# Optimization experiments

Measured on AMD Instinct MI355X. Metric: run time of the kernel, lower is better.

The kernel has to match this reference:

```python
import jax, jax.numpy as jnp
import numpy as np

NUM_GRAPHS = 512
NODES_PER_GRAPH = 152  # hard-coded by reshape(-1, 152*C) in the original forward
DEG = 8
N = NUM_GRAPHS * NODES_PER_GRAPH          # 77824
E = NUM_GRAPHS * NODES_PER_GRAPH * DEG    # 622592
F_IN = 128
HID = 32
HEADS = 6
C = HID * HEADS                           # 192
EPS = 1e-5
NEG_SLOPE = 0.2


def setup_inputs() -> dict:
    key = jax.random.key(0)
    ks = jax.random.split(key, 20)
    x = jax.random.normal(ks[0], (N, F_IN), dtype=jnp.float32)
    # edges are intra-graph: local indices in [0,152) + per-graph offset
    src_l = jax.random.randint(ks[1], (E,), 0, NODES_PER_GRAPH)
    dst_l = jax.random.randint(ks[2], (E,), 0, NODES_PER_GRAPH)
    offs = (jnp.arange(E) // (NODES_PER_GRAPH * DEG)) * NODES_PER_GRAPH
    edge_index = jnp.stack([src_l + offs, dst_l + offs]).astype(jnp.int32)
    batch = (jnp.arange(N) // NODES_PER_GRAPH).astype(jnp.int32)

    def g(k, shape, s=0.05):
        return jax.random.normal(k, shape, dtype=jnp.float32) * s

    return {
        "x": x, "edge_index": edge_index, "batch": batch,
        # GATConv 1: in=128 -> heads=6, d_head=32, concat -> 192
        "W1": g(ks[3], (F_IN, C)), "a_src1": g(ks[4], (HEADS, HID)),
        "a_dst1": g(ks[5], (HEADS, HID)), "b1": jnp.zeros((C,), jnp.float32),
        # GATConv 2: in=192 -> 192
        "W2": g(ks[6], (C, C)), "a_src2": g(ks[7], (HEADS, HID)),
        "a_dst2": g(ks[8], (HEADS, HID)), "b2": jnp.zeros((C,), jnp.float32),
        # GraphNorm 1 / 2: weight, bias, mean_scale (all init like PyG: 1,0,1)
        "gw1": jnp.ones((C,), jnp.float32), "gb1": jnp.zeros((C,), jnp.float32),
        "gms1": jnp.ones((C,), jnp.float32),
        "gw2": jnp.ones((C,), jnp.float32), "gb2": jnp.zeros((C,), jnp.float32),
        "gms2": jnp.ones((C,), jnp.float32),
    }


def _gat_conv(x, W, a_src, a_dst, bias, src, dst):
    # PyG GATConv (concat=True, negative_slope=0.2, add_self_loops already in src/dst)
    h = (x @ W).reshape(N, HEADS, HID)                      # [N,H,D]
    al_s = jnp.einsum('nhd,hd->nh', h, a_src)               # [N,H]
    al_d = jnp.einsum('nhd,hd->nh', h, a_dst)
    e = jax.nn.leaky_relu(al_s[src] + al_d[dst], NEG_SLOPE)  # [E',H]
    # segment softmax over incoming edges of each dst node
    m = jax.ops.segment_max(e, dst, num_segments=N)
    ex = jnp.exp(e - m[dst])
    denom = jax.ops.segment_sum(ex, dst, num_segments=N)
    alpha = ex / denom[dst]                                  # [E',H]
    out = jax.ops.segment_sum(alpha[:, :, None] * h[src], dst, num_segments=N)
    return out.reshape(N, C) + bias


def _graph_norm(x, batch, w, b, ms):
    # PyG GraphNorm: x - mean_scale*mean, normalized by per-graph std
    cnt = jax.ops.segment_sum(jnp.ones((N, 1), x.dtype), batch, num_segments=NUM_GRAPHS)
    mean = jax.ops.segment_sum(x, batch, num_segments=NUM_GRAPHS) / cnt
    out = x - mean[batch] * ms
    var = jax.ops.segment_sum(out * out, batch, num_segments=NUM_GRAPHS) / cnt
    return out / jnp.sqrt(var[batch] + EPS) * w + b


def reference(x, edge_index, batch, W1, a_src1, a_dst1, b1, W2, a_src2, a_dst2, b2,
              gw1, gb1, gms1, gw2, gb2, gms2):
    # add self loops (PyG GATConv default)
    loops = jnp.arange(N, dtype=edge_index.dtype)
    src = jnp.concatenate([edge_index[0], loops])
    dst = jnp.concatenate([edge_index[1], loops])

    h = _gat_conv(x, W1, a_src1, a_dst1, b1, src, dst)
    h = jax.nn.elu(h)
    h = _graph_norm(h, batch, gw1, gb1, gms1)
    # dropout p=0.5 is identity in eval mode
    h = _gat_conv(h, W2, a_src2, a_dst2, b2, src, dst)
    h = jax.nn.elu(h)
    h = _graph_norm(h, batch, gw2, gb2, gms2)
    out = h.reshape(-1, NODES_PER_GRAPH * C)  # [512, 152*192]
    return out  # original returns (x, embedding) where embedding is x itself
```

## Files before the change

kernel.cpp:

```cpp
#include <hip/hip_runtime.h>
#include <stdint.h>

#define NGRAPH 512
#define NPG    152
#define NNODES (NGRAPH*NPG)
#define DEG    8
#define EPG    (NPG*DEG)
#define NEDGE  (NNODES*DEG)
#define CCH    192
#define HEADS  6
#define HID    32
#define NSEG   (NPG+EPG)
#define HSTR   36

typedef __attribute__((ext_vector_type(8))) short short8v;
typedef __attribute__((ext_vector_type(4))) float f32x4;
typedef __attribute__((ext_vector_type(4))) unsigned short ushort4v;

__device__ __forceinline__ unsigned short f2bf(float f){
  union { float f; uint32_t u; } x; x.f = f;
  uint32_t u = x.u;
  return (unsigned short)((u + 0x7fffu + ((u >> 16) & 1u)) >> 16);
}
__device__ __forceinline__ float bitsf(uint32_t b){
  union { uint32_t u; float f; } x; x.u = b; return x.f;
}
__device__ __forceinline__ void gload_lds16(const void* g, void* l){
  __builtin_amdgcn_global_load_lds((const __attribute__((address_space(1))) void*)g,
                                   (__attribute__((address_space(3))) void*)l, 16, 0, 0);
}

__global__ void wprep_all(const float* __restrict__ W1, const float* __restrict__ W2,
                          unsigned short* __restrict__ Wt1, unsigned short* __restrict__ Wt2){
  int idx = blockIdx.x*256 + threadIdx.x;
  if (idx < CCH*128){
    int c = idx >> 7, k = idx & 127;
    Wt1[idx] = f2bf(W1[k*CCH + c]);
  } else if (idx < CCH*(128+192)){
    int j = idx - CCH*128;
    int c = j/192, k = j - c*192;
    Wt2[j] = f2bf(W2[k*CCH + c]);
  }
}

template<int K, bool A_BF16>
__global__ __launch_bounds__(256) void gemm_mfma(const void* __restrict__ Ap,
    const unsigned short* __restrict__ Bt, unsigned short* __restrict__ H){
  __shared__ unsigned short lA[64*K];
  __shared__ unsigned short lB[96*K];
  const int t  = threadIdx.x;
  const int m0 = blockIdx.x*64, c0 = blockIdx.y*96;

  if (A_BF16){
    const unsigned short* A = (const unsigned short*)Ap + (size_t)m0*K;
    const int CH = 64*K/8;
    for (int i=t; i<CH; i+=256){
      int o   = i*16;
      int row = o / (2*K);
      int db  = o - row*(2*K);
      int sc  = (db>>4) ^ (row&7);
      gload_lds16(A + (size_t)row*K + sc*8, lA + (size_t)(i-(t&63))*8);
    }
  } else {
    const float* A = (const float*)Ap;
    const int KC = K/8;
    for (int i=t; i<64*KC; i+=256){
      int row = i/KC, c8 = i - row*KC;
      const float* p = A + (size_t)(m0+row)*K + c8*8;
      float4 v0 = *(const float4*)p;
      float4 v1 = *(const float4*)(p+4);
      short8v pk;
      pk[0]=(short)f2bf(v0.x); pk[1]=(short)f2bf(v0.y); pk[2]=(short)f2bf(v0.z); pk[3]=(short)f2bf(v0.w);
      pk[4]=(short)f2bf(v1.x); pk[5]=(short)f2bf(v1.y); pk[6]=(short)f2bf(v1.z); pk[7]=(short)f2bf(v1.w);
      *(short8v*)((char*)lA + row*(2*K) + ((c8*16) ^ ((row&7)<<4))) = pk;
    }
  }
  {
    const unsigned short* Bg = Bt + (size_t)c0*K;
    const int CH = 96*K/8;
    for (int i=t; i<CH; i+=256){
      int o   = i*16;
      int row = o / (2*K);
      int db  = o - row*(2*K);
      int sc  = (db>>4) ^ (row&7);
      gload_lds16(Bg + (size_t)row*K + sc*8, lB + (size_t)(i-(t&63))*8);
    }
  }
  __syncthreads();

  const int wid = t>>6, l = t&63;
  const int wr = wid>>1, wc = wid&1;
  const int r16 = l&15, kq = l>>4;
  f32x4 acc[2][3] = {};
  #pragma unroll
  for (int kk=0; kk<K/32; kk++){
    const int chunk = kk*4 + kq;
    short8v af[2], bf[3];
    #pragma unroll
    for (int m=0;m<2;m++){
      int row = wr*32 + m*16 + r16;
      af[m] = *(const short8v*)((const char*)lA + row*(2*K) + ((chunk*16) ^ ((row&7)<<4)));
    }
    #pragma unroll
    for (int n=0;n<3;n++){
      int col = wc*48 + n*16 + r16;
      bf[n] = *(const short8v*)((const char*)lB + col*(2*K) + ((chunk*16) ^ ((col&7)<<4)));
    }
    #pragma unroll
    for (int m=0;m<2;m++)
      #pragma unroll
      for (int n=0;n<3;n++)
        acc[m][n] = __builtin_amdgcn_mfma_f32_16x16x32_bf16(af[m], bf[n], acc[m][n], 0,0,0);
  }
  const int crow = (l>>4)*4;
  #pragma unroll
  for (int m=0;m<2;m++){
    #pragma unroll
    for (int n=0;n<3;n++){
      int colg = c0 + wc*48 + n*16 + r16;
      #pragma unroll
      for (int r=0;r<4;r++){
        int rowg = m0 + wr*32 + m*16 + crow + r;
        H[(size_t)rowg*CCH + colg] = f2bf(acc[m][n][r]);
      }
    }
  }
}

template<bool OUT_BF16>
__global__ __launch_bounds__(256) void gat_edge(
    const unsigned short* __restrict__ H,
    const int* __restrict__ esrc, const int* __restrict__ edst,
    const float* __restrict__ a_src, const float* __restrict__ a_dst,
    const float* __restrict__ bias, const float* __restrict__ gw,
    const float* __restrict__ gb, const float* __restrict__ gms,
    void* __restrict__ OUTp)
{
  __shared__ float hN[NPG*HSTR];
  __shared__ float score[NSEG];
  __shared__ int   ssrc[NSEG];
  __shared__ int   cnt[256];
  __shared__ int   woff[NPG];
  __shared__ float als[NPG], ald[NPG];
  __shared__ float4 ps[8][8];
  __shared__ float4 mred4[8], vred4[8];

  const int t    = threadIdx.x;
  const int g    = blockIdx.x & 511;
  const int hd   = blockIdx.x >> 9;
  const int base = g*NPG;
  const int lane32 = t & 31, grp = t >> 5;

  cnt[t] = (t < NPG) ? 1 : 0;

  for (int i=t; i<NPG*4; i+=256){
    int n = i>>2, c8c = i&3;
    int4 v = *(const int4*)(H + (size_t)(base+n)*CCH + hd*HID + c8c*8);
    uint32_t w0=(uint32_t)v.x, w1=(uint32_t)v.y, w2=(uint32_t)v.z, w3=(uint32_t)v.w;
    float* dst = &hN[n*HSTR + c8c*8];
    float4 lo = { bitsf(w0<<16), bitsf(w0&0xffff0000u), bitsf(w1<<16), bitsf(w1&0xffff0000u) };
    float4 hi = { bitsf(w2<<16), bitsf(w2&0xffff0000u), bitsf(w3<<16), bitsf(w3&0xffff0000u) };
    *(float4*)dst = lo;
    *(float4*)(dst+4) = hi;
  }
  __syncthreads();

  for (int i=t; i<EPG; i+=256){
    int d = edst[g*EPG + i] - base;
    atomicAdd(&cnt[d], 1);
  }
  const float avs = a_src[hd*HID + lane32];
  const float avd = a_dst[hd*HID + lane32];
  #pragma unroll
  for (int k=0;k<19;k++){
    int n = grp + (k<<3);
    float hv = hN[n*HSTR + lane32];
    float s1 = hv*avs, s2 = hv*avd;
    #pragma unroll
    for (int m=16;m>0;m>>=1){ s1 += __shfl_xor(s1, m, 32); s2 += __shfl_xor(s2, m, 32); }
    if (lane32==0){ als[n]=s1; ald[n]=s2; }
  }
  __syncthreads();

  for (int off=1; off<256; off<<=1){
    int a = cnt[t];
    int b = (t>=off) ? cnt[t-off] : 0;
    __syncthreads();
    cnt[t] = a + b;
    __syncthreads();
  }
  if (t<NPG) woff[t] = (t==0) ? 0 : cnt[t-1];
  __syncthreads();

  for (int i=t; i<EPG; i+=256){
    int s = esrc[g*EPG + i] - base;
    int d = edst[g*EPG + i] - base;
    float e = als[s] + ald[d];
    e = (e>0.f) ? e : 0.2f*e;
    int pos = atomicAdd(&woff[d], 1);
    score[pos] = __expf(e); ssrc[pos] = s;
  }
  if (t < NPG){
    float e = als[t] + ald[t];
    e = (e>0.f) ? e : 0.2f*e;
    int pos = atomicAdd(&woff[t], 1);
    score[pos] = __expf(e); ssrc[pos] = t;
  }
  __syncthreads();

  const int sub = (lane32>>3)&3;
  const int c8  = lane32&7;
  const int o   = grp*4 + sub;
  float4 acc[5]; float den[5]; int stq[5], lnq[5];
  #pragma unroll
  for (int q=0;q<5;q++){
    int n = o + q*32;
    int st=0, en=0;
    if (n < NPG){ st = (n==0)?0:cnt[n-1]; en = cnt[n]; }
    stq[q]=st; lnq[q]=en-st;
    acc[q] = float4{0.f,0.f,0.f,0.f}; den[q]=0.f;
  }
  #pragma unroll
  for (int q=0;q<5;q++){
    int st=stq[q], len=lnq[q];
    int rounds = (len+3)>>2;
    for (int r=0;r<rounds;++r){
      #pragma unroll
      for (int u=0;u<4;u++){
        int j = r*4+u;
        int idx = st + ((j<len)? j : 0);
        float ex = score[idx];
        if (j>=len) ex = 0.f;
        int s = ssrc[idx];
        const float4 hv = *(const float4*)&hN[s*HSTR + c8*4];
        den[q] += ex;
        acc[q].x = fmaf(ex, hv.x, acc[q].x);
        acc[q].y = fmaf(ex, hv.y, acc[q].y);
        acc[q].z = fmaf(ex, hv.z, acc[q].z);
        acc[q].w = fmaf(ex, hv.w, acc[q].w);
      }
    }
  }

  const int cb = hd*HID + c8*4;
  const float4 bs4 = *(const float4*)&bias[cb];
  const float4 gw4 = *(const float4*)&gw[cb];
  const float4 gb4 = *(const float4*)&gb[cb];
  const float4 ms4 = *(const float4*)&gms[cb];

  float4 outv[5];
  float4 psum = {0.f,0.f,0.f,0.f};
  #pragma unroll
  for (int q=0;q<5;q++){
    int n = o + q*32;
    float4 x = {0.f,0.f,0.f,0.f};
    if (n < NPG){
      float inv = 1.f/den[q];
      x.x = acc[q].x*inv + bs4.x;  x.y = acc[q].y*inv + bs4.y;
      x.z = acc[q].z*inv + bs4.z;  x.w = acc[q].w*inv + bs4.w;
      x.x = (x.x>0.f)?x.x:(__expf(x.x)-1.f);
      x.y = (x.y>0.f)?x.y:(__expf(x.y)-1.f);
      x.z = (x.z>0.f)?x.z:(__expf(x.z)-1.f);
      x.w = (x.w>0.f)?x.w:(__expf(x.w)-1.f);
      psum.x+=x.x; psum.y+=x.y; psum.z+=x.z; psum.w+=x.w;
    }
    outv[q]=x;
  }
  psum.x += __shfl_xor(psum.x, 8, 32); psum.y += __shfl_xor(psum.y, 8, 32);
  psum.z += __shfl_xor(psum.z, 8, 32); psum.w += __shfl_xor(psum.w, 8, 32);
  psum.x += __shfl_xor(psum.x,16, 32); psum.y += __shfl_xor(psum.y,16, 32);
  psum.z += __shfl_xor(psum.z,16, 32); psum.w += __shfl_xor(psum.w,16, 32);
  if (sub==0) ps[grp][c8] = psum;
  __syncthreads();
  if (t < 8){
    float4 m = {0.f,0.f,0.f,0.f};
    #pragma unroll
    for (int q=0;q<8;q++){ float4 v=ps[q][t]; m.x+=v.x; m.y+=v.y; m.z+=v.z; m.w+=v.w; }
    m.x*=(1.f/152.f); m.y*=(1.f/152.f); m.z*=(1.f/152.f); m.w*=(1.f/152.f);
    mred4[t] = m;
  }
  __syncthreads();
  const float4 mean4 = mred4[c8];
  float4 v2 = {0.f,0.f,0.f,0.f};
  #pragma unroll
  for (int q=0;q<5;q++){
    int n = o + q*32;
    if (n < NPG){
      outv[q].x -= mean4.x*ms4.x; outv[q].y -= mean4.y*ms4.y;
      outv[q].z -= mean4.z*ms4.z; outv[q].w -= mean4.w*ms4.w;
      v2.x = fmaf(outv[q].x,outv[q].x,v2.x); v2.y = fmaf(outv[q].y,outv[q].y,v2.y);
      v2.z = fmaf(outv[q].z,outv[q].z,v2.z); v2.w = fmaf(outv[q].w,outv[q].w,v2.w);
    }
  }
  v2.x += __shfl_xor(v2.x, 8, 32); v2.y += __shfl_xor(v2.y, 8, 32);
  v2.z += __shfl_xor(v2.z, 8, 32); v2.w += __shfl_xor(v2.w, 8, 32);
  v2.x += __shfl_xor(v2.x,16, 32); v2.y += __shfl_xor(v2.y,16, 32);
  v2.z += __shfl_xor(v2.z,16, 32); v2.w += __shfl_xor(v2.w,16, 32);
  if (sub==0) ps[grp][c8] = v2;
  __syncthreads();
  if (t < 8){
    float4 s = {0.f,0.f,0.f,0.f};
    #pragma unroll
    for (int q=0;q<8;q++){ float4 v=ps[q][t]; s.x+=v.x; s.y+=v.y; s.z+=v.z; s.w+=v.w; }
    float4 rv;
    rv.x = rsqrtf(s.x*(1.f/152.f)+1e-5f); rv.y = rsqrtf(s.y*(1.f/152.f)+1e-5f);
    rv.z = rsqrtf(s.z*(1.f/152.f)+1e-5f); rv.w = rsqrtf(s.w*(1.f/152.f)+1e-5f);
    vred4[t] = rv;
  }
  __syncthreads();
  const float4 rs4 = vred4[c8];
  #pragma unroll
  for (int q=0;q<5;q++){
    int n = o + q*32;
    if (n < NPG){
      float4 x = outv[q];
      x.x = x.x*rs4.x*gw4.x + gb4.x;  x.y = x.y*rs4.y*gw4.y + gb4.y;
      x.z = x.z*rs4.z*gw4.z + gb4.z;  x.w = x.w*rs4.w*gw4.w + gb4.w;
      size_t oidx = (size_t)(base+n)*CCH + cb;
      if (OUT_BF16){
        ushort4v pk = { f2bf(x.x), f2bf(x.y), f2bf(x.z), f2bf(x.w) };
        *(ushort4v*)((unsigned short*)OUTp + oidx) = pk;
      } else {
        *(float4*)((float*)OUTp + oidx) = x;
      }
    }
  }
}

extern "C" void kernel_launch(void* const* d_in, const int* in_sizes, int n_in,
                              void* d_out, int out_size, void* d_ws, size_t ws_size,
                              hipStream_t stream){
  (void)in_sizes; (void)n_in; (void)out_size; (void)ws_size;
  const float* x    = (const float*)d_in[0];
  const int*   ei   = (const int*)  d_in[1];
  const float* W1   = (const float*)d_in[3];
  const float* as1  = (const float*)d_in[4];
  const float* ad1  = (const float*)d_in[5];
  const float* b1   = (const float*)d_in[6];
  const float* W2   = (const float*)d_in[7];
  const float* as2  = (const float*)d_in[8];
  const float* ad2  = (const float*)d_in[9];
  const float* b2   = (const float*)d_in[10];
  const float* gw1  = (const float*)d_in[11];
  const float* gb1  = (const float*)d_in[12];
  const float* gms1 = (const float*)d_in[13];
  const float* gw2  = (const float*)d_in[14];
  const float* gb2  = (const float*)d_in[15];
  const float* gms2 = (const float*)d_in[16];
  const int* esrc = ei;
  const int* edst = ei + NEDGE;

  char* ws = (char*)d_ws;
  unsigned short* Hbuf = (unsigned short*)ws;
  unsigned short* Obuf = (unsigned short*)(ws + (size_t)NNODES*CCH*2);
  unsigned short* Wt1  = (unsigned short*)(ws + (size_t)NNODES*CCH*4);
  unsigned short* Wt2  = Wt1 + CCH*128;

  wprep_all<<<(CCH*(128+192)+255)/256, 256, 0, stream>>>(W1, W2, Wt1, Wt2);

  gemm_mfma<128,false><<<dim3(NNODES/64,2), 256, 0, stream>>>((const void*)x, Wt1, Hbuf);
  gat_edge<true><<<NGRAPH*HEADS, 256, 0, stream>>>(Hbuf, esrc, edst, as1, ad1, b1, gw1, gb1, gms1, (void*)Obuf);
  gemm_mfma<192,true><<<dim3(NNODES/64,2), 256, 0, stream>>>((const void*)Obuf, Wt2, Hbuf);
  gat_edge<false><<<NGRAPH*HEADS, 256, 0, stream>>>(Hbuf, esrc, edst, as2, ad2, b2, gw2, gb2, gms2, d_out);
}
```

Before: 285.9 us.

## Build per-graph CSR once and compute attention scores inline in GAT kernels

Adds a csr_build kernel that, once per graph, sorts edges by destination into a compact 16-bit source list plus offsets. Both GAT edge kernels previously redid this histogram, scan and scatter for every one of the 6 heads. Each gat_edge block now loads the prebuilt CSR with direct global-to-LDS loads. It computes the attention logit and exp inline during aggregation instead of staging them in a score array, and fuses the als/ald dot products into the H load. This removes repeated atomics, scan barriers and edge-index reads, but recomputes exp per channel-lane and adds an extra launch and workspace.

Measured after the change: 232.8 us. 1.23x faster.

```diff
diff --git a/kernel.cpp b/kernel.cpp
--- a/kernel.cpp
+++ b/kernel.cpp
@@ -12,6 +12,7 @@
 #define HID    32
 #define NSEG   (NPG+EPG)
 #define HSTR   36
+#define CNTP   160
 
 typedef __attribute__((ext_vector_type(8))) short short8v;
 typedef __attribute__((ext_vector_type(4))) float f32x4;
@@ -41,6 +42,60 @@
     int c = j/192, k = j - c*192;
     Wt2[j] = f2bf(W2[k*CCH + c]);
   }
+}
+
+__global__ __launch_bounds__(256) void csr_build(const int* __restrict__ esrc,
+    const int* __restrict__ edst, unsigned short* __restrict__ gsrc,
+    int* __restrict__ gcnt){
+  __shared__ int cnt[256];
+  __shared__ int woff[NPG];
+  __shared__ __align__(16) unsigned short slots[NSEG];
+  const int t = threadIdx.x, g = blockIdx.x, base = g*NPG;
+
+  cnt[t] = (t < NPG) ? 1 : 0;
+  __syncthreads();
+
+  int es[5], ed[5];
+  #pragma unroll
+  for (int u=0;u<5;u++){
+    int i = t + u*256;
+    if (i < EPG){
+      es[u] = esrc[g*EPG + i] - base;
+      ed[u] = edst[g*EPG + i] - base;
+      atomicAdd(&cnt[ed[u]], 1);
+    }
+  }
+  __syncthreads();
+  for (int off=1; off<256; off<<=1){
+    int a = cnt[t];
+    int b = (t>=off) ? cnt[t-off] : 0;
+    __syncthreads();
+    cnt[t] = a + b;
+    __syncthreads();
+  }
+  if (t < NPG){
+    int st = (t==0) ? 0 : cnt[t-1];
+    woff[t] = st;
+    gcnt[g*CNTP + t] = st;
+  } else if (t < CNTP){
+    gcnt[g*CNTP + t] = NSEG;
+  }
+  __syncthreads();
+  #pragma unroll
+  for (int u=0;u<5;u++){
+    int i = t + u*256;
+    if (i < EPG){
+      int pos = atomicAdd(&woff[ed[u]], 1);
+      slots[pos] = (unsigned short)es[u];
+    }
+  }
+  if (t < NPG){
+    int pos = atomicAdd(&woff[t], 1);
+    slots[pos] = (unsigned short)t;
+  }
+  __syncthreads();
+  for (int i=t; i<NSEG/8; i+=256)
+    *(int4*)(gsrc + (size_t)g*NSEG + i*8) = *(const int4*)&slots[i*8];
 }
 
 template<int K, bool A_BF16>
@@ -130,18 +185,16 @@
 template<bool OUT_BF16>
 __global__ __launch_bounds__(256) void gat_edge(
     const unsigned short* __restrict__ H,
-    const int* __restrict__ esrc, const int* __restrict__ edst,
+    const unsigned short* __restrict__ gsrc, const int* __restrict__ gcnt,
     const float* __restrict__ a_src, const float* __restrict__ a_dst,
     const float* __restrict__ bias, const float* __restrict__ gw,
     const float* __restrict__ gb, const float* __restrict__ gms,
     void* __restrict__ OUTp)
 {
   __shared__ float hN[NPG*HSTR];
-  __shared__ float score[NSEG];
-  __shared__ int   ssrc[NSEG];
-  __shared__ int   cnt[256];
-  __shared__ int   woff[NPG];
   __shared__ float als[NPG], ald[NPG];
+  __shared__ __align__(16) unsigned short lsrc[NSEG];
+  __shared__ __align__(16) int lcnt[CNTP];
   __shared__ float4 ps[8][8];
   __shared__ float4 mred4[8], vred4[8];
 
@@ -151,87 +204,70 @@
   const int base = g*NPG;
   const int lane32 = t & 31, grp = t >> 5;
 
-  cnt[t] = (t < NPG) ? 1 : 0;
-
-  for (int i=t; i<NPG*4; i+=256){
-    int n = i>>2, c8c = i&3;
-    int4 v = *(const int4*)(H + (size_t)(base+n)*CCH + hd*HID + c8c*8);
-    uint32_t w0=(uint32_t)v.x, w1=(uint32_t)v.y, w2=(uint32_t)v.z, w3=(uint32_t)v.w;
-    float* dst = &hN[n*HSTR + c8c*8];
-    float4 lo = { bitsf(w0<<16), bitsf(w0&0xffff0000u), bitsf(w1<<16), bitsf(w1&0xffff0000u) };
-    float4 hi = { bitsf(w2<<16), bitsf(w2&0xffff0000u), bitsf(w3<<16), bitsf(w3&0xffff0000u) };
-    *(float4*)dst = lo;
-    *(float4*)(dst+4) = hi;
-  }
-  __syncthreads();
-
-  for (int i=t; i<EPG; i+=256){
-    int d = edst[g*EPG + i] - base;
-    atomicAdd(&cnt[d], 1);
-  }
-  const float avs = a_src[hd*HID + lane32];
-  const float avd = a_dst[hd*HID + lane32];
-  #pragma unroll
-  for (int k=0;k<19;k++){
-    int n = grp + (k<<3);
-    float hv = hN[n*HSTR + lane32];
-    float s1 = hv*avs, s2 = hv*avd;
-    #pragma unroll
-    for (int m=16;m>0;m>>=1){ s1 += __shfl_xor(s1, m, 32); s2 += __shfl_xor(s2, m, 32); }
-    if (lane32==0){ als[n]=s1; ald[n]=s2; }
-  }
-  __syncthreads();
-
-  for (int off=1; off<256; off<<=1){
-    int a = cnt[t];
-    int b = (t>=off) ? cnt[t-off] : 0;
-    __syncthreads();
-    cnt[t] = a + b;
-    __syncthreads();
-  }
-  if (t<NPG) woff[t] = (t==0) ? 0 : cnt[t-1];
-  __syncthreads();
-
-  for (int i=t; i<EPG; i+=256){
-    int s = esrc[g*EPG + i] - base;
-    int d = edst[g*EPG + i] - base;
-    float e = als[s] + ald[d];
-    e = (e>0.f) ? e : 0.2f*e;
-    int pos = atomicAdd(&woff[d], 1);
-    score[pos] = __expf(e); ssrc[pos] = s;
-  }
-  if (t < NPG){
-    float e = als[t] + ald[t];
-    e = (e>0.f) ? e : 0.2f*e;
-    int pos = atomicAdd(&woff[t], 1);
-    score[pos] = __expf(e); ssrc[pos] = t;
+  {
+    const unsigned short* gs = gsrc + (size_t)g*NSEG;
+    for (int i=t; i<NSEG/8; i+=256)
+      gload_lds16(gs + i*8, lsrc + (size_t)(i-(t&63))*8);
+    const int* gc = gcnt + (size_t)g*CNTP;
+    if (t < CNTP/4)
+      gload_lds16(gc + t*4, lcnt + (size_t)(t-(t&63))*4);
+  }
+
+  const int c8c = t&3, nb = t>>2;
+  const int ab = hd*HID + c8c*8;
+  const float4 avs0 = *(const float4*)&a_src[ab];
+  const float4 avs1 = *(const float4*)&a_src[ab+4];
+  const float4 avd0 = *(const float4*)&a_dst[ab];
+  const float4 avd1 = *(const float4*)&a_dst[ab+4];
+  #pragma unroll
+  for (int it=0; it<3; it++){
+    int n = nb + it*64;
+    if (n < NPG){
+      int4 v = *(const int4*)(H + (size_t)(base+n)*CCH + hd*HID + c8c*8);
+      uint32_t w0=(uint32_t)v.x, w1=(uint32_t)v.y, w2=(uint32_t)v.z, w3=(uint32_t)v.w;
+      float4 lo = { bitsf(w0<<16), bitsf(w0&0xffff0000u), bitsf(w1<<16), bitsf(w1&0xffff0000u) };
+      float4 hi = { bitsf(w2<<16), bitsf(w2&0xffff0000u), bitsf(w3<<16), bitsf(w3&0xffff0000u) };
+      float* dst = &hN[n*HSTR + c8c*8];
+      *(float4*)dst = lo;
+      *(float4*)(dst+4) = hi;
+      float s1 = lo.x*avs0.x + lo.y*avs0.y + lo.z*avs0.z + lo.w*avs0.w
+               + hi.x*avs1.x + hi.y*avs1.y + hi.z*avs1.z + hi.w*avs1.w;
+      float s2 = lo.x*avd0.x + lo.y*avd0.y + lo.z*avd0.z + lo.w*avd0.w
+               + hi.x*avd1.x + hi.y*avd1.y + hi.z*avd1.z + hi.w*avd1.w;
+      s1 += __shfl_xor(s1, 1); s1 += __shfl_xor(s1, 2);
+      s2 += __shfl_xor(s2, 1); s2 += __shfl_xor(s2, 2);
+      if (c8c == 0){ als[n] = s1; ald[n] = s2; }
+    }
   }
   __syncthreads();
 
   const int sub = (lane32>>3)&3;
   const int c8  = lane32&7;
   const int o   = grp*4 + sub;
-  float4 acc[5]; float den[5]; int stq[5], lnq[5];
+  float4 acc[5]; float den[5]; int stq[5], lnq[5]; float aldn[5];
   #pragma unroll
   for (int q=0;q<5;q++){
     int n = o + q*32;
-    int st=0, en=0;
-    if (n < NPG){ st = (n==0)?0:cnt[n-1]; en = cnt[n]; }
-    stq[q]=st; lnq[q]=en-st;
+    int st=0, en=0; float ad=0.f;
+    if (n < NPG){ st = lcnt[n]; en = lcnt[n+1]; ad = ald[n]; }
+    stq[q]=st; lnq[q]=en-st; aldn[q]=ad;
     acc[q] = float4{0.f,0.f,0.f,0.f}; den[q]=0.f;
   }
   #pragma unroll
   for (int q=0;q<5;q++){
     int st=stq[q], len=lnq[q];
+    float ad = aldn[q];
     int rounds = (len+3)>>2;
     for (int r=0;r<rounds;++r){
       #pragma unroll
       for (int u=0;u<4;u++){
         int j = r*4+u;
         int idx = st + ((j<len)? j : 0);
-        float ex = score[idx];
+        int s = (int)lsrc[idx];
+        float e = als[s] + ad;
+        e = (e>0.f) ? e : 0.2f*e;
+        float ex = __expf(e);
         if (j>=len) ex = 0.f;
-        int s = ssrc[idx];
         const float4 hv = *(const float4*)&hN[s*HSTR + c8*4];
         den[q] += ex;
         acc[q].x = fmaf(ex, hv.x, acc[q].x);
@@ -355,11 +391,14 @@
   unsigned short* Obuf = (unsigned short*)(ws + (size_t)NNODES*CCH*2);
   unsigned short* Wt1  = (unsigned short*)(ws + (size_t)NNODES*CCH*4);
   unsigned short* Wt2  = Wt1 + CCH*128;
-
+  unsigned short* gsrc = Wt2 + CCH*192;
+  int*            gcnt = (int*)(gsrc + (size_t)NGRAPH*NSEG);
+
+  csr_build<<<NGRAPH, 256, 0, stream>>>(esrc, edst, gsrc, gcnt);
   wprep_all<<<(CCH*(128+192)+255)/256, 256, 0, stream>>>(W1, W2, Wt1, Wt2);
 
   gemm_mfma<128,false><<<dim3(NNODES/64,2), 256, 0, stream>>>((const void*)x, Wt1, Hbuf);
-  gat_edge<true><<<NGRAPH*HEADS, 256, 0, stream>>>(Hbuf, esrc, edst, as1, ad1, b1, gw1, gb1, gms1, (void*)Obuf);
+  gat_edge<true><<<NGRAPH*HEADS, 256, 0, stream>>>(Hbuf, gsrc, gcnt, as1, ad1, b1, gw1, gb1, gms1, (void*)Obuf);
   gemm_mfma<192,true><<<dim3(NNODES/64,2), 256, 0, stream>>>((const void*)Obuf, Wt2, Hbuf);
-  gat_edge<false><<<NGRAPH*HEADS, 256, 0, stream>>>(Hbuf, esrc, edst, as2, ad2, b2, gw2, gb2, gms2, d_out);
-}
+  gat_edge<false><<<NGRAPH*HEADS, 256, 0, stream>>>(Hbuf, gsrc, gcnt, as2, ad2, b2, gw2, gb2, gms2, d_out);
+}
```
